# Kernel tuning notes

Hardware: AMD Instinct MI355X
Metric: run time of the kernel (lower is better)

The kernel has to match this reference:

```python
import jax, jax.numpy as jnp
import numpy as np

EPS = 1e-6

def _ln(x, g, b):
    mu = jnp.mean(x, -1, keepdims=True)
    var = jnp.mean((x - mu) ** 2, -1, keepdims=True)
    return (x - mu) / jnp.sqrt(var + EPS) * g + b

def _attn(q, k, v, nh, mask=None):
    B, Lq, H = q.shape
    Lk = k.shape[1]
    dh = H // nh
    q = q.reshape(B, Lq, nh, dh).transpose(0, 2, 1, 3)
    k = k.reshape(B, Lk, nh, dh).transpose(0, 2, 1, 3)
    v = v.reshape(B, Lk, nh, dh).transpose(0, 2, 1, 3)
    s = jnp.einsum('bhqd,bhkd->bhqk', q, k) * (1.0 / np.float32(np.sqrt(dh)))
    if mask is not None:
        s = jnp.where(mask, jnp.float32(-1e30), s)
    a = jax.nn.softmax(s, axis=-1)
    o = jnp.einsum('bhqk,bhkd->bhqd', a, v)
    return o.transpose(0, 2, 1, 3).reshape(B, Lq, H)

def _forward(byte_seq, patch_boundaries, emb, g_ln1_g, g_ln1_b, g_wqkv, g_bqkv, g_wo, g_bo,
             g_ln2_g, g_ln2_b, g_w1, g_b1, g_w2, g_b2, fn_g, fn_b,
             ca_ln_g, ca_ln_b, ca_wqkv, ca_bqkv, ca_wo, ca_bo, head_w, head_b,
             n_heads=16, ca_heads=8):
    B, S = byte_seq.shape
    P = patch_boundaries.shape[1]
    H = emb.shape[1]
    x = emb[byte_seq]  # [B,S,H] byte embeddings (local encoder)
    # ragged patch pooling: patch id of byte i = #boundaries <= i (BabylonIndex patches)
    pos = jnp.arange(S)
    pid = jax.vmap(lambda bd: jnp.searchsorted(bd, pos, side='right'))(patch_boundaries)
    pid = jnp.clip(pid, 0, P - 1)
    seg = lambda vals, ids: jax.ops.segment_sum(vals, ids, num_segments=P)
    sums = jax.vmap(seg)(x, pid)                                  # [B,P,H]
    cnts = jax.vmap(seg)(jnp.ones((B, S), x.dtype), pid)          # [B,P]
    patches = sums / jnp.maximum(cnts, 1.0)[..., None]            # mean-pooled patch reps
    causal = jnp.triu(jnp.ones((P, P), bool), 1)
    def layer(h, p):
        l1g, l1b, wqkv, bqkv, wo, bo, l2g, l2b, w1, b1, w2, b2 = p
        n = _ln(h, l1g, l1b)
        q, k, v = jnp.split(n @ wqkv + bqkv, 3, axis=-1)
        h = h + _attn(q, k, v, n_heads, causal) @ wo + bo
        n2 = _ln(h, l2g, l2b)
        h = h + jax.nn.gelu(n2 @ w1 + b1, approximate=False) @ w2 + b2
        return h, None
    patches, _ = jax.lax.scan(layer, patches, (g_ln1_g, g_ln1_b, g_wqkv, g_bqkv, g_wo, g_bo,
                                               g_ln2_g, g_ln2_b, g_w1, g_b1, g_w2, g_b2))
    patches = _ln(patches, fn_g, fn_b)  # GlobalLatentTransformer.final_norm
    # cross attention: byte queries attend to global patch representations
    qn = _ln(x, ca_ln_g, ca_ln_b)
    kvn = _ln(patches, ca_ln_g, ca_ln_b)
    q = qn @ ca_wqkv[:, :H] + ca_bqkv[:H]
    k = kvn @ ca_wqkv[:, H:2 * H] + ca_bqkv[H:2 * H]
    v = kvn @ ca_wqkv[:, 2 * H:] + ca_bqkv[2 * H:]
    h = x + _attn(q, k, v, ca_heads) @ ca_wo + ca_bo
    return h @ head_w + head_b  # [B,S,256] next-byte logits

def setup_inputs() -> dict:
    key = jax.random.key(0)
    ks = jax.random.split(key, 16)
    B, S, P, H, L, V = 2, 4096, 256, 1024, 4, 256
    std = 0.02
    d = {}
    d['byte_seq'] = jax.random.randint(ks[0], (B, S), 0, V, dtype=jnp.int32)
    d['patch_boundaries'] = jnp.sort(jax.random.randint(ks[1], (B, P), 1, S, dtype=jnp.int32), axis=-1)
    d['emb'] = jax.random.normal(ks[2], (V, H), jnp.float32) * std
    d['g_ln1_g'] = jnp.ones((L, H), jnp.float32)
    d['g_ln1_b'] = jnp.zeros((L, H), jnp.float32)
    d['g_wqkv'] = jax.random.normal(ks[3], (L, H, 3 * H), jnp.float32) * std
    d['g_bqkv'] = jnp.zeros((L, 3 * H), jnp.float32)
    d['g_wo'] = jax.random.normal(ks[4], (L, H, H), jnp.float32) * std
    d['g_bo'] = jnp.zeros((L, H), jnp.float32)
    d['g_ln2_g'] = jnp.ones((L, H), jnp.float32)
    d['g_ln2_b'] = jnp.zeros((L, H), jnp.float32)
    d['g_w1'] = jax.random.normal(ks[5], (L, H, 4 * H), jnp.float32) * std
    d['g_b1'] = jnp.zeros((L, 4 * H), jnp.float32)
    d['g_w2'] = jax.random.normal(ks[6], (L, 4 * H, H), jnp.float32) * std
    d['g_b2'] = jnp.zeros((L, H), jnp.float32)
    d['fn_g'] = jnp.ones((H,), jnp.float32)
    d['fn_b'] = jnp.zeros((H,), jnp.float32)
    d['ca_ln_g'] = jnp.ones((H,), jnp.float32)
    d['ca_ln_b'] = jnp.zeros((H,), jnp.float32)
    d['ca_wqkv'] = jax.random.normal(ks[7], (H, 3 * H), jnp.float32) * std
    d['ca_bqkv'] = jnp.zeros((3 * H,), jnp.float32)
    d['ca_wo'] = jax.random.normal(ks[8], (H, H), jnp.float32) * std
    d['ca_bo'] = jnp.zeros((H,), jnp.float32)
    d['head_w'] = jax.random.normal(ks[9], (H, V), jnp.float32) * std
    d['head_b'] = jnp.zeros((V,), jnp.float32)
    return d

def reference(byte_seq, patch_boundaries, emb, g_ln1_g, g_ln1_b, g_wqkv, g_bqkv, g_wo, g_bo,
              g_ln2_g, g_ln2_b, g_w1, g_b1, g_w2, g_b2, fn_g, fn_b,
              ca_ln_g, ca_ln_b, ca_wqkv, ca_bqkv, ca_wo, ca_bo, head_w, head_b):
    return _forward(byte_seq, patch_boundaries, emb, g_ln1_g, g_ln1_b, g_wqkv, g_bqkv, g_wo, g_bo,
                    g_ln2_g, g_ln2_b, g_w1, g_b1, g_w2, g_b2, fn_g, fn_b,
                    ca_ln_g, ca_ln_b, ca_wqkv, ca_bqkv, ca_wo, ca_bo, head_w, head_b)
```

## Files before the change

### kernel.cpp

```cpp
#include <hip/hip_runtime.h>
#include <hip/hip_bf16.h>
#include <math.h>

#define Hdim 1024
#define Bsz  2
#define Slen 4096
#define Pn   256
#define NLAY 4

typedef __attribute__((ext_vector_type(8))) __bf16 bfrag;
typedef __attribute__((ext_vector_type(4))) float  f32x4;

__device__ __forceinline__ float gelu_exact(float x) {
  return 0.5f * x * (1.0f + erff(x * 0.70710678118654752f));
}
__device__ __forceinline__ short f2b(float x) {
  __hip_bfloat16 h = __float2bfloat16(x);
  return *reinterpret_cast<short*>(&h);
}

__global__ void embed_kernel(const int* __restrict__ seq, const float* __restrict__ emb,
                             float* __restrict__ x) {
  int row = blockIdx.x;
  int tid = threadIdx.x;
  int tok = seq[row];
  float4 v = *(const float4*)(emb + (size_t)tok * Hdim + tid * 4);
  *(float4*)(x + (size_t)row * Hdim + tid * 4) = v;
}

__global__ void pid_kernel(const int* __restrict__ bounds, int* __restrict__ pid) {
  int i = blockIdx.x * 256 + threadIdx.x;
  int b = i >> 12;
  int s = i & (Slen - 1);
  const int* bd = bounds + b * Pn;
  int lo = 0, hi = Pn;
  while (lo < hi) { int m = (lo + hi) >> 1; if (bd[m] <= s) lo = m + 1; else hi = m; }
  pid[i] = min(lo, Pn - 1);
}

__global__ void pool_kernel(const float* __restrict__ x, const int* __restrict__ pid,
                            float* __restrict__ patches) {
  int bp = blockIdx.x;
  int b = bp >> 8;
  int p = bp & (Pn - 1);
  const int* pv = pid + b * Slen;
  int lo = 0, hi = Slen;
  while (lo < hi) { int m = (lo + hi) >> 1; if (pv[m] < p) lo = m + 1; else hi = m; }
  int start = lo;
  lo = 0; hi = Slen;
  while (lo < hi) { int m = (lo + hi) >> 1; if (pv[m] < p + 1) lo = m + 1; else hi = m; }
  int end = lo;
  int tid = threadIdx.x;
  float4 acc = {0.f, 0.f, 0.f, 0.f};
  for (int s = start; s < end; ++s) {
    float4 xv = *(const float4*)(x + ((size_t)(b * Slen + s)) * Hdim + tid * 4);
    acc.x += xv.x; acc.y += xv.y; acc.z += xv.z; acc.w += xv.w;
  }
  float cnt = (float)(end - start);
  float r = 1.0f / fmaxf(cnt, 1.0f);
  float4 o = {acc.x * r, acc.y * r, acc.z * r, acc.w * r};
  *(float4*)(patches + (size_t)bp * Hdim + tid * 4) = o;
}

template<int OBF>
__global__ void ln_kernel(const float* __restrict__ in, const float* __restrict__ g,
                          const float* __restrict__ bvec, void* __restrict__ outv) {
  int row = blockIdx.x;
  int tid = threadIdx.x;
  const float* xr = in + (size_t)row * Hdim;
  float4 v = *(const float4*)(xr + tid * 4);
  float s  = v.x + v.y + v.z + v.w;
  float ss = v.x * v.x + v.y * v.y + v.z * v.z + v.w * v.w;
#pragma unroll
  for (int off = 32; off; off >>= 1) { s += __shfl_xor(s, off); ss += __shfl_xor(ss, off); }
  __shared__ float rs[4], rss[4];
  int wid = tid >> 6;
  if ((tid & 63) == 0) { rs[wid] = s; rss[wid] = ss; }
  __syncthreads();
  float tot  = rs[0] + rs[1] + rs[2] + rs[3];
  float tot2 = rss[0] + rss[1] + rss[2] + rss[3];
  float mu = tot * (1.0f / Hdim);
  float var = tot2 * (1.0f / Hdim) - mu * mu;
  float rstd = rsqrtf(var + 1e-6f);
  float4 gg = *(const float4*)(g + tid * 4);
  float4 bb = *(const float4*)(bvec + tid * 4);
  float4 r;
  r.x = (v.x - mu) * rstd * gg.x + bb.x;
  r.y = (v.y - mu) * rstd * gg.y + bb.y;
  r.z = (v.z - mu) * rstd * gg.z + bb.z;
  r.w = (v.w - mu) * rstd * gg.w + bb.w;
  if (OBF) {
    short4 o; o.x = f2b(r.x); o.y = f2b(r.y); o.z = f2b(r.z); o.w = f2b(r.w);
    *(short4*)((short*)outv + (size_t)row * Hdim + tid * 4) = o;
  } else {
    *(float4*)((float*)outv + (size_t)row * Hdim + tid * 4) = r;
  }
}

__global__ void wconv_kernel(const float* __restrict__ in, short* __restrict__ out,
                             int ldin, int K, size_t in_lstride, size_t out_lstride) {
  int z = blockIdx.z;
  const float* src = in + (size_t)z * in_lstride;
  short* dst = out + (size_t)z * out_lstride;
  int n0 = blockIdx.x * 32, k0 = blockIdx.y * 32;
  int tx = threadIdx.x & 31, ty = threadIdx.x >> 5;
  __shared__ float t[32][33];
#pragma unroll
  for (int i = 0; i < 4; i++)
    t[ty + 8 * i][tx] = src[(size_t)(k0 + ty + 8 * i) * ldin + n0 + tx];
  __syncthreads();
#pragma unroll
  for (int i = 0; i < 4; i++)
    dst[(size_t)(n0 + ty + 8 * i) * K + k0 + tx] = f2b(t[tx][ty + 8 * i]);
}

__global__ void vt_kernel(const float* __restrict__ in, short* __restrict__ out) {
  int bh = blockIdx.z; int h = bh & 7; int b = bh >> 3;
  int kk0 = blockIdx.x * 32, d0 = blockIdx.y * 32;
  int tx = threadIdx.x & 31, ty = threadIdx.x >> 5;
  __shared__ float t[32][33];
  const float* src = in + (size_t)b * Pn * Hdim + h * 128;
#pragma unroll
  for (int i = 0; i < 4; i++)
    t[ty + 8 * i][tx] = src[(size_t)(kk0 + ty + 8 * i) * Hdim + d0 + tx];
  __syncthreads();
  short* dst = out + (size_t)bh * 128 * 256;
#pragma unroll
  for (int i = 0; i < 4; i++)
    dst[(size_t)(d0 + ty + 8 * i) * 256 + kk0 + tx] = f2b(t[tx][ty + 8 * i]);
}

__global__ void vtg_kernel(const short* __restrict__ qkvb, short* __restrict__ out) {
  int bh = blockIdx.z; int h = bh & 15; int b = bh >> 4;
  int kk0 = blockIdx.x * 32, d0 = blockIdx.y * 32;
  int tx = threadIdx.x & 31, ty = threadIdx.x >> 5;
  __shared__ short t[32][33];
  const short* src = qkvb + (size_t)b * Pn * 3072 + 2048 + h * 64;
#pragma unroll
  for (int i = 0; i < 4; i++)
    t[ty + 8 * i][tx] = src[(size_t)(kk0 + ty + 8 * i) * 3072 + d0 + tx];
  __syncthreads();
  short* dst = out + (size_t)bh * 64 * 256;
#pragma unroll
  for (int i = 0; i < 4; i++)
    dst[(size_t)(d0 + ty + 8 * i) * 256 + kk0 + tx] = t[tx][ty + 8 * i];
}

template<int EPI, int OBF>
__launch_bounds__(256)
__global__ void gemm_bf16(const short* __restrict__ A, const short* __restrict__ Bt,
                          const float* __restrict__ bias, const float* __restrict__ res,
                          void* __restrict__ Cv, int ldc, int K) {
  __shared__ short As[128][40];
  __shared__ short Bs[128][40];
  int tid = threadIdx.x;
  int n0 = blockIdx.x * 128, m0 = blockIdx.y * 128;
  int lr = tid >> 2;
  int lc = (tid & 3) * 8;
  int wid = tid >> 6, lane = tid & 63;
  int wm = (wid & 1) * 64, wn = (wid >> 1) * 64;
  int quad = lane >> 4, l16 = lane & 15;
  f32x4 acc[4][4];
#pragma unroll
  for (int i = 0; i < 4; i++)
#pragma unroll
    for (int j = 0; j < 4; j++) acc[i][j] = (f32x4){0.f, 0.f, 0.f, 0.f};

  for (int k0 = 0; k0 < K; k0 += 32) {
    int4 av0 = *(const int4*)(A + (size_t)(m0 + lr) * K + k0 + lc);
    int4 av1 = *(const int4*)(A + (size_t)(m0 + lr + 64) * K + k0 + lc);
    int4 bv0 = *(const int4*)(Bt + (size_t)(n0 + lr) * K + k0 + lc);
    int4 bv1 = *(const int4*)(Bt + (size_t)(n0 + lr + 64) * K + k0 + lc);
    __syncthreads();
    *(int4*)&As[lr][lc] = av0;  *(int4*)&As[lr + 64][lc] = av1;
    *(int4*)&Bs[lr][lc] = bv0;  *(int4*)&Bs[lr + 64][lc] = bv1;
    __syncthreads();
    bfrag af[4], bfv[4];
#pragma unroll
    for (int mi = 0; mi < 4; mi++)
      af[mi] = *reinterpret_cast<const bfrag*>(&As[wm + mi * 16 + l16][quad * 8]);
#pragma unroll
    for (int ni = 0; ni < 4; ni++)
      bfv[ni] = *reinterpret_cast<const bfrag*>(&Bs[wn + ni * 16 + l16][quad * 8]);
#pragma unroll
    for (int mi = 0; mi < 4; mi++)
#pragma unroll
      for (int ni = 0; ni < 4; ni++)
        acc[mi][ni] = __builtin_amdgcn_mfma_f32_16x16x32_bf16(af[mi], bfv[ni], acc[mi][ni], 0, 0, 0);
  }

#pragma unroll
  for (int mi = 0; mi < 4; mi++)
#pragma unroll
    for (int ni = 0; ni < 4; ni++) {
      int c = n0 + wn + ni * 16 + l16;
      float bsv = bias[c];
#pragma unroll
      for (int reg = 0; reg < 4; reg++) {
        int r = m0 + wm + mi * 16 + quad * 4 + reg;
        float v = acc[mi][ni][reg] + bsv;
        if (EPI == 1) v = gelu_exact(v);
        if (EPI == 2) v += res[(size_t)r * ldc + c];
        if (OBF) ((short*)Cv)[(size_t)r * ldc + c] = f2b(v);
        else     ((float*)Cv)[(size_t)r * ldc + c] = v;
      }
    }
}

template<int EPI, int OBF>
__launch_bounds__(256)
__global__ void gemm_bf16_64(const short* __restrict__ A, const short* __restrict__ Bt,
                             const float* __restrict__ bias, const float* __restrict__ res,
                             void* __restrict__ Cv, int ldc, int K) {
  __shared__ short As[64][40];
  __shared__ short Bs[64][40];
  int tid = threadIdx.x;
  int n0 = blockIdx.x * 64, m0 = blockIdx.y * 64;
  int lr = tid >> 2;
  int lc = (tid & 3) * 8;
  int wid = tid >> 6, lane = tid & 63;
  int wm = (wid & 1) * 32, wn = (wid >> 1) * 32;
  int quad = lane >> 4, l16 = lane & 15;
  f32x4 acc[2][2];
#pragma unroll
  for (int i = 0; i < 2; i++)
#pragma unroll
    for (int j = 0; j < 2; j++) acc[i][j] = (f32x4){0.f, 0.f, 0.f, 0.f};

  for (int k0 = 0; k0 < K; k0 += 32) {
    int4 av = *(const int4*)(A + (size_t)(m0 + lr) * K + k0 + lc);
    int4 bv = *(const int4*)(Bt + (size_t)(n0 + lr) * K + k0 + lc);
    __syncthreads();
    *(int4*)&As[lr][lc] = av;
    *(int4*)&Bs[lr][lc] = bv;
    __syncthreads();
    bfrag af[2], bfv[2];
#pragma unroll
    for (int mi = 0; mi < 2; mi++)
      af[mi] = *reinterpret_cast<const bfrag*>(&As[wm + mi * 16 + l16][quad * 8]);
#pragma unroll
    for (int ni = 0; ni < 2; ni++)
      bfv[ni] = *reinterpret_cast<const bfrag*>(&Bs[wn + ni * 16 + l16][quad * 8]);
#pragma unroll
    for (int mi = 0; mi < 2; mi++)
#pragma unroll
      for (int ni = 0; ni < 2; ni++)
        acc[mi][ni] = __builtin_amdgcn_mfma_f32_16x16x32_bf16(af[mi], bfv[ni], acc[mi][ni], 0, 0, 0);
  }

#pragma unroll
  for (int mi = 0; mi < 2; mi++)
#pragma unroll
    for (int ni = 0; ni < 2; ni++) {
      int c = n0 + wn + ni * 16 + l16;
      float bsv = bias[c];
#pragma unroll
      for (int reg = 0; reg < 4; reg++) {
        int r = m0 + wm + mi * 16 + quad * 4 + reg;
        float v = acc[mi][ni][reg] + bsv;
        if (EPI == 1) v = gelu_exact(v);
        if (EPI == 2) v += res[(size_t)r * ldc + c];
        if (OBF) ((short*)Cv)[(size_t)r * ldc + c] = f2b(v);
        else     ((float*)Cv)[(size_t)r * ldc + c] = v;
      }
    }
}

__launch_bounds__(256)
__global__ void gemm_splitk(const short* __restrict__ A, const short* __restrict__ Bt,
                            float* __restrict__ part, int K, int Ks) {
  __shared__ short As[64][40];
  __shared__ short Bs[64][40];
  int tid = threadIdx.x;
  int n0 = blockIdx.x * 64, m0 = blockIdx.y * 64, s = blockIdx.z;
  int kbase = s * Ks;
  int lr = tid >> 2;
  int lc = (tid & 3) * 8;
  int wid = tid >> 6, lane = tid & 63;
  int wm = (wid & 1) * 32, wn = (wid >> 1) * 32;
  int quad = lane >> 4, l16 = lane & 15;
  f32x4 acc[2][2];
#pragma unroll
  for (int i = 0; i < 2; i++)
#pragma unroll
    for (int j = 0; j < 2; j++) acc[i][j] = (f32x4){0.f, 0.f, 0.f, 0.f};

  for (int k0 = kbase; k0 < kbase + Ks; k0 += 32) {
    int4 av = *(const int4*)(A + (size_t)(m0 + lr) * K + k0 + lc);
    int4 bv = *(const int4*)(Bt + (size_t)(n0 + lr) * K + k0 + lc);
    __syncthreads();
    *(int4*)&As[lr][lc] = av;
    *(int4*)&Bs[lr][lc] = bv;
    __syncthreads();
    bfrag af[2], bfv[2];
#pragma unroll
    for (int mi = 0; mi < 2; mi++)
      af[mi] = *reinterpret_cast<const bfrag*>(&As[wm + mi * 16 + l16][quad * 8]);
#pragma unroll
    for (int ni = 0; ni < 2; ni++)
      bfv[ni] = *reinterpret_cast<const bfrag*>(&Bs[wn + ni * 16 + l16][quad * 8]);
#pragma unroll
    for (int mi = 0; mi < 2; mi++)
#pragma unroll
      for (int ni = 0; ni < 2; ni++)
        acc[mi][ni] = __builtin_amdgcn_mfma_f32_16x16x32_bf16(af[mi], bfv[ni], acc[mi][ni], 0, 0, 0);
  }

#pragma unroll
  for (int mi = 0; mi < 2; mi++)
#pragma unroll
    for (int ni = 0; ni < 2; ni++) {
      int c = n0 + wn + ni * 16 + l16;
#pragma unroll
      for (int reg = 0; reg < 4; reg++) {
        int r = m0 + wm + mi * 16 + quad * 4 + reg;
        part[(size_t)s * 524288 + (size_t)r * 1024 + c] = acc[mi][ni][reg];
      }
    }
}

__global__ void w2red_kernel(const float* __restrict__ part, const float* __restrict__ bias,
                             float* __restrict__ patches) {
  int i = (blockIdx.x * 256 + threadIdx.x) * 4;
  float4 v = *(const float4*)(part + i);
#pragma unroll
  for (int s = 1; s < 4; s++) {
    float4 p = *(const float4*)(part + (size_t)s * 524288 + i);
    v.x += p.x; v.y += p.y; v.z += p.z; v.w += p.w;
  }
  int c = i & 1023;
  float4 bv = *(const float4*)(bias + c);
  float4 rv = *(const float4*)(patches + i);
  v.x += bv.x + rv.x; v.y += bv.y + rv.y; v.z += bv.z + rv.z; v.w += bv.w + rv.w;
  *(float4*)(patches + i) = v;
}

__launch_bounds__(256)
__global__ void attn_global3(const short* __restrict__ qkvb, const short* __restrict__ vtg,
                             short* __restrict__ outp) {
  int qt = blockIdx.x;
  int bh = blockIdx.y; int h = bh & 15, b = bh >> 4;
  int tid = threadIdx.x;
  int wid = tid >> 6, lane = tid & 63;
  int quad = lane >> 4, l16 = lane & 15;
  int q0 = qt * 64 + wid * 16;
  __shared__ short KV[64 * 72];
  __shared__ short Pl[4][16][264];
  const short* qrow = qkvb + ((size_t)(b * Pn + q0 + l16)) * 3072 + h * 64 + quad * 8;
  bfrag qf[2];
#pragma unroll
  for (int kd = 0; kd < 2; kd++) qf[kd] = *(const bfrag*)(qrow + kd * 32);
  f32x4 sacc[16];
#pragma unroll
  for (int n = 0; n < 16; n++) sacc[n] = (f32x4){0.f, 0.f, 0.f, 0.f};
  int cr = tid >> 2, cc = (tid & 3) * 16;
#pragma unroll
  for (int kc = 0; kc < 4; kc++) {
    if (kc <= qt) {
      const short* ksrc = qkvb + ((size_t)(b * Pn + kc * 64 + cr)) * 3072 + 1024 + h * 64 + cc;
      int4 v0 = *(const int4*)(ksrc);
      int4 v1 = *(const int4*)(ksrc + 8);
      __syncthreads();
      *(int4*)&KV[cr * 72 + cc] = v0;
      *(int4*)&KV[cr * 72 + cc + 8] = v1;
      __syncthreads();
#pragma unroll
      for (int n = 0; n < 4; n++)
#pragma unroll
        for (int kd = 0; kd < 2; kd++) {
          bfrag kf = *(const bfrag*)&KV[(n * 16 + l16) * 72 + kd * 32 + quad * 8];
          sacc[kc * 4 + n] = __builtin_amdgcn_mfma_f32_16x16x32_bf16(qf[kd], kf, sacc[kc * 4 + n], 0, 0, 0);
        }
    }
  }
  int nfr = (qt + 1) * 4;
  const float scale = 0.125f;
  float mx[4] = {-1e30f, -1e30f, -1e30f, -1e30f};
#pragma unroll
  for (int n = 0; n < 16; n++) {
    if (n < nfr) {
      int col = n * 16 + l16;
#pragma unroll
      for (int r = 0; r < 4; r++)
        if (col <= q0 + quad * 4 + r) mx[r] = fmaxf(mx[r], sacc[n][r]);
    }
  }
#pragma unroll
  for (int off = 1; off < 16; off <<= 1)
#pragma unroll
    for (int r = 0; r < 4; r++) mx[r] = fmaxf(mx[r], __shfl_xor(mx[r], off));
  float ls[4] = {0.f, 0.f, 0.f, 0.f};
#pragma unroll
  for (int n = 0; n < 16; n++) {
    if (n < nfr) {
      int col = n * 16 + l16;
#pragma unroll
      for (int r = 0; r < 4; r++) {
        float p = (col <= q0 + quad * 4 + r) ? __expf((sacc[n][r] - mx[r]) * scale) : 0.f;
        Pl[wid][quad * 4 + r][col] = f2b(p);
        ls[r] += p;
      }
    }
  }
#pragma unroll
  for (int off = 1; off < 16; off <<= 1)
#pragma unroll
    for (int r = 0; r < 4; r++) ls[r] += __shfl_xor(ls[r], off);
  float rl[4];
#pragma unroll
  for (int r = 0; r < 4; r++) rl[r] = 1.0f / ls[r];

  f32x4 oacc[4];
#pragma unroll
  for (int n = 0; n < 4; n++) oacc[n] = (f32x4){0.f, 0.f, 0.f, 0.f};
#pragma unroll
  for (int kc = 0; kc < 4; kc++) {
    if (kc <= qt) {
      const short* vsrc = vtg + (size_t)bh * 64 * 256 + cr * 256 + kc * 64 + cc;
      int4 v0 = *(const int4*)(vsrc);
      int4 v1 = *(const int4*)(vsrc + 8);
      __syncthreads();
      *(int4*)&KV[cr * 72 + cc] = v0;
      *(int4*)&KV[cr * 72 + cc + 8] = v1;
      __syncthreads();
#pragma unroll
      for (int kk = 0; kk < 2; kk++) {
        bfrag pa = *(const bfrag*)&Pl[wid][l16][kc * 64 + kk * 32 + quad * 8];
#pragma unroll
        for (int n = 0; n < 4; n++) {
          bfrag vf = *(const bfrag*)&KV[(n * 16 + l16) * 72 + kk * 32 + quad * 8];
          oacc[n] = __builtin_amdgcn_mfma_f32_16x16x32_bf16(pa, vf, oacc[n], 0, 0, 0);
        }
      }
    }
  }
#pragma unroll
  for (int n = 0; n < 4; n++)
#pragma unroll
    for (int r = 0; r < 4; r++)
      outp[(size_t)(b * Pn + q0 + quad * 4 + r) * Hdim + h * 64 + n * 16 + l16] = f2b(oacc[n][r] * rl[r]);
}

__launch_bounds__(256)
__global__ void attn_cross4(const short* __restrict__ q, const short* __restrict__ k,
                            const short* __restrict__ vt, short* __restrict__ outp) {
  int bh = blockIdx.y; int h = bh & 7, b = bh >> 3;
  int tid = threadIdx.x;
  int wid = tid >> 6, lane = tid & 63;
  int quad = lane >> 4, l16 = lane & 15;
  int q0 = blockIdx.x * 64 + wid * 16;
  __shared__ short KV[9216];
  __shared__ short Pl[4][16][264];
  const short* qrow = q + ((size_t)(b * Slen + q0 + l16)) * Hdim + h * 128 + quad * 8;
  bfrag qf[4];
#pragma unroll
  for (int kd = 0; kd < 4; kd++) qf[kd] = *(const bfrag*)(qrow + kd * 32);
  f32x4 sacc[16];
#pragma unroll
  for (int n = 0; n < 16; n++) sacc[n] = (f32x4){0.f, 0.f, 0.f, 0.f};

  int cr4 = tid >> 2, cc4 = (tid & 3) * 32;
#pragma unroll
  for (int kc = 0; kc < 4; kc++) {
    const short* ksrc = k + ((size_t)(b * Pn + kc * 64 + cr4)) * Hdim + h * 128 + cc4;
    int4 v0 = *(const int4*)(ksrc);
    int4 v1 = *(const int4*)(ksrc + 8);
    int4 v2 = *(const int4*)(ksrc + 16);
    int4 v3 = *(const int4*)(ksrc + 24);
    __syncthreads();
    *(int4*)&KV[cr4 * 136 + cc4]      = v0;
    *(int4*)&KV[cr4 * 136 + cc4 + 8]  = v1;
    *(int4*)&KV[cr4 * 136 + cc4 + 16] = v2;
    *(int4*)&KV[cr4 * 136 + cc4 + 24] = v3;
    __syncthreads();
#pragma unroll
    for (int n = 0; n < 4; n++)
#pragma unroll
      for (int kd = 0; kd < 4; kd++) {
        bfrag kf = *(const bfrag*)&KV[(n * 16 + l16) * 136 + kd * 32 + quad * 8];
        sacc[kc * 4 + n] = __builtin_amdgcn_mfma_f32_16x16x32_bf16(qf[kd], kf, sacc[kc * 4 + n], 0, 0, 0);
      }
  }

  const float scale = 0.088388347648318447f;
  float mx[4] = {-1e30f, -1e30f, -1e30f, -1e30f};
#pragma unroll
  for (int n = 0; n < 16; n++)
#pragma unroll
    for (int r = 0; r < 4; r++) mx[r] = fmaxf(mx[r], sacc[n][r]);
#pragma unroll
  for (int off = 1; off < 16; off <<= 1)
#pragma unroll
    for (int r = 0; r < 4; r++) mx[r] = fmaxf(mx[r], __shfl_xor(mx[r], off));
  float ls[4] = {0.f, 0.f, 0.f, 0.f};
#pragma unroll
  for (int n = 0; n < 16; n++)
#pragma unroll
    for (int r = 0; r < 4; r++) {
      float p = __expf((sacc[n][r] - mx[r]) * scale);
      Pl[wid][quad * 4 + r][n * 16 + l16] = f2b(p);
      ls[r] += p;
    }
#pragma unroll
  for (int off = 1; off < 16; off <<= 1)
#pragma unroll
    for (int r = 0; r < 4; r++) ls[r] += __shfl_xor(ls[r], off);
  float rl[4];
#pragma unroll
  for (int r = 0; r < 4; r++) rl[r] = 1.0f / ls[r];

  f32x4 oacc[8];
#pragma unroll
  for (int n = 0; n < 8; n++) oacc[n] = (f32x4){0.f, 0.f, 0.f, 0.f};
  int cr2 = tid >> 1, cc2 = (tid & 1) * 32;
#pragma unroll
  for (int kc = 0; kc < 4; kc++) {
    const short* vsrc = vt + (size_t)bh * 32768 + cr2 * 256 + kc * 64 + cc2;
    int4 v0 = *(const int4*)(vsrc);
    int4 v1 = *(const int4*)(vsrc + 8);
    int4 v2 = *(const int4*)(vsrc + 16);
    int4 v3 = *(const int4*)(vsrc + 24);
    __syncthreads();
    *(int4*)&KV[cr2 * 72 + cc2]      = v0;
    *(int4*)&KV[cr2 * 72 + cc2 + 8]  = v1;
    *(int4*)&KV[cr2 * 72 + cc2 + 16] = v2;
    *(int4*)&KV[cr2 * 72 + cc2 + 24] = v3;
    __syncthreads();
#pragma unroll
    for (int kk = 0; kk < 2; kk++) {
      bfrag pa = *(const bfrag*)&Pl[wid][l16][kc * 64 + kk * 32 + quad * 8];
#pragma unroll
      for (int n = 0; n < 8; n++) {
        bfrag vf = *(const bfrag*)&KV[(n * 16 + l16) * 72 + kk * 32 + quad * 8];
        oacc[n] = __builtin_amdgcn_mfma_f32_16x16x32_bf16(pa, vf, oacc[n], 0, 0, 0);
      }
    }
  }
#pragma unroll
  for (int n = 0; n < 8; n++)
#pragma unroll
    for (int r = 0; r < 4; r++)
      outp[(size_t)(b * Slen + q0 + quad * 4 + r) * Hdim + h * 128 + n * 16 + l16] = f2b(oacc[n][r] * rl[r]);
}

extern "C" void kernel_launch(void* const* d_in, const int* in_sizes, int n_in,
                              void* d_out, int out_size, void* d_ws, size_t ws_size,
                              hipStream_t stream) {
  const int*   byte_seq = (const int*)d_in[0];
  const int*   pbound   = (const int*)d_in[1];
  const float* emb      = (const float*)d_in[2];
  const float* g_ln1_g  = (const float*)d_in[3];
  const float* g_ln1_b  = (const float*)d_in[4];
  const float* g_wqkv   = (const float*)d_in[5];
  const float* g_bqkv   = (const float*)d_in[6];
  const float* g_wo     = (const float*)d_in[7];
  const float* g_bo     = (const float*)d_in[8];
  const float* g_ln2_g  = (const float*)d_in[9];
  const float* g_ln2_b  = (const float*)d_in[10];
  const float* g_w1     = (const float*)d_in[11];
  const float* g_b1     = (const float*)d_in[12];
  const float* g_w2     = (const float*)d_in[13];
  const float* g_b2     = (const float*)d_in[14];
  const float* fn_g     = (const float*)d_in[15];
  const float* fn_b     = (const float*)d_in[16];
  const float* ca_ln_g  = (const float*)d_in[17];
  const float* ca_ln_b  = (const float*)d_in[18];
  const float* ca_wqkv  = (const float*)d_in[19];
  const float* ca_bqkv  = (const float*)d_in[20];
  const float* ca_wo    = (const float*)d_in[21];
  const float* ca_bo    = (const float*)d_in[22];
  const float* head_w   = (const float*)d_in[23];
  const float* head_b   = (const float*)d_in[24];
  float* out = (float*)d_out;

  float* x       = (float*)d_ws;
  float* patches = x + 8388608;
  float* vbuf    = patches + 524288;
  float* w2part  = vbuf + 524288;
  int*   pid     = (int*)(w2part + 2097152);
  short* nbuf    = (short*)(pid + 8192);
  short* attn_o  = nbuf + 524288;
  short* mid     = attn_o + 524288;
  short* qn      = mid + 2097152;
  short* qb      = qn + 8388608;
  short* xb      = qb + 8388608;
  short* kb      = xb + 8388608;
  short* vt      = kb + 524288;
  short* qkvb    = vt + 524288;
  short* vtg     = qkvb + 1572864;
  short* wqkv_t  = vtg + 524288;
  short* wo_t    = wqkv_t + 12582912;
  short* w1_t    = wo_t + 4194304;
  short* w2_t    = w1_t + 16777216;
  short* caq_t   = w2_t + 16777216;
  short* cak_t   = caq_t + 1048576;
  short* cav_t   = cak_t + 1048576;
  short* cawo_t  = cav_t + 1048576;
  short* head_t  = cawo_t + 1048576;
  short* caout   = qn;

  embed_kernel<<<Bsz * Slen, 256, 0, stream>>>(byte_seq, emb, x);
  pid_kernel<<<(Bsz * Slen) / 256, 256, 0, stream>>>(pbound, pid);
  pool_kernel<<<Bsz * Pn, 256, 0, stream>>>(x, pid, patches);

  wconv_kernel<<<dim3(96, 32, 4), 256, 0, stream>>>(g_wqkv, wqkv_t, 3072, 1024, 3145728, 3145728);
  wconv_kernel<<<dim3(32, 32, 4), 256, 0, stream>>>(g_wo, wo_t, 1024, 1024, 1048576, 1048576);
  wconv_kernel<<<dim3(128, 32, 4), 256, 0, stream>>>(g_w1, w1_t, 4096, 1024, 4194304, 4194304);
  wconv_kernel<<<dim3(32, 128, 4), 256, 0, stream>>>(g_w2, w2_t, 1024, 4096, 4194304, 4194304);
  wconv_kernel<<<dim3(32, 32, 3), 256, 0, stream>>>(ca_wqkv, caq_t, 3072, 1024, 1024, 1048576);
  wconv_kernel<<<dim3(32, 32, 1), 256, 0, stream>>>(ca_wo, cawo_t, 1024, 1024, 0, 0);
  wconv_kernel<<<dim3(8, 32, 1), 256, 0, stream>>>(head_w, head_t, 256, 1024, 0, 0);

  for (int l = 0; l < NLAY; ++l) {
    ln_kernel<1><<<Bsz * Pn, 256, 0, stream>>>(patches, g_ln1_g + l * Hdim, g_ln1_b + l * Hdim, nbuf);
    gemm_bf16_64<0, 1><<<dim3(48, 8), 256, 0, stream>>>(
        nbuf, wqkv_t + (size_t)l * 3145728, g_bqkv + l * 3072, nullptr, qkvb, 3072, 1024);
    vtg_kernel<<<dim3(8, 2, 32), 256, 0, stream>>>(qkvb, vtg);
    attn_global3<<<dim3(4, 32), 256, 0, stream>>>(qkvb, vtg, attn_o);
    gemm_bf16_64<2, 0><<<dim3(16, 8), 256, 0, stream>>>(
        attn_o, wo_t + (size_t)l * 1048576, g_bo + l * Hdim, patches, patches, 1024, 1024);
    ln_kernel<1><<<Bsz * Pn, 256, 0, stream>>>(patches, g_ln2_g + l * Hdim, g_ln2_b + l * Hdim, nbuf);
    gemm_bf16_64<1, 1><<<dim3(64, 8), 256, 0, stream>>>(
        nbuf, w1_t + (size_t)l * 4194304, g_b1 + l * 4096, nullptr, mid, 4096, 1024);
    gemm_splitk<<<dim3(16, 8, 4), 256, 0, stream>>>(
        mid, w2_t + (size_t)l * 4194304, w2part, 4096, 1024);
    w2red_kernel<<<512, 256, 0, stream>>>(w2part, g_b2 + l * Hdim, patches);
  }

  ln_kernel<0><<<Bsz * Pn, 256, 0, stream>>>(patches, fn_g, fn_b, patches);
  ln_kernel<1><<<Bsz * Pn, 256, 0, stream>>>(patches, ca_ln_g, ca_ln_b, nbuf);

  gemm_bf16_64<0, 1><<<dim3(16, 8), 256, 0, stream>>>(
      nbuf, cak_t, ca_bqkv + 1024, nullptr, kb, 1024, 1024);
  gemm_bf16_64<0, 0><<<dim3(16, 8), 256, 0, stream>>>(
      nbuf, cav_t, ca_bqkv + 2048, nullptr, vbuf, 1024, 1024);
  vt_kernel<<<dim3(8, 4, 16), 256, 0, stream>>>(vbuf, vt);

  ln_kernel<1><<<Bsz * Slen, 256, 0, stream>>>(x, ca_ln_g, ca_ln_b, qn);
  gemm_bf16<0, 1><<<dim3(8, 64), 256, 0, stream>>>(
      qn, caq_t, ca_bqkv, nullptr, qb, 1024, 1024);

  attn_cross4<<<dim3(64, 16), 256, 0, stream>>>(qb, kb, vt, caout);

  gemm_bf16<2, 1><<<dim3(8, 64), 256, 0, stream>>>(
      caout, cawo_t, ca_bo, x, xb, 1024, 1024);

  gemm_bf16_64<0, 0><<<dim3(4, 128), 256, 0, stream>>>(
      xb, head_t, head_b, nullptr, out, 256, 1024);
}
```

Before: 850.4 us.

## Load GEMM tiles directly to LDS and fuse cross-attn LayerNorm into embedding

All three bf16 GEMM kernels now stage A and B tiles with global_load_lds (direct global-to-LDS 16-byte loads) into unpadded 32-wide LDS rows, so the data no longer passes through registers. The byte-level LayerNorm for cross-attention queries is folded into the embedding kernel, which removes a separate pass over the 8192x1024 activation. Dropping the LDS padding can raise bank conflicts on fragment reads, and the LayerNorm now uses a single-pass E[x^2]-mu^2 variance, which is slightly less numerically robust.

```diff
diff --git a/kernel.cpp b/kernel.cpp
--- a/kernel.cpp
+++ b/kernel.cpp
@@ -18,14 +18,41 @@
   __hip_bfloat16 h = __float2bfloat16(x);
   return *reinterpret_cast<short*>(&h);
 }
-
-__global__ void embed_kernel(const int* __restrict__ seq, const float* __restrict__ emb,
-                             float* __restrict__ x) {
+__device__ __forceinline__ void gload16(const short* g, short* l) {
+  __builtin_amdgcn_global_load_lds(
+      (const __attribute__((address_space(1))) unsigned int*)g,
+      (__attribute__((address_space(3))) unsigned int*)l, 16, 0, 0);
+}
+
+__global__ void embed_ln_kernel(const int* __restrict__ seq, const float* __restrict__ emb,
+                                const float* __restrict__ g, const float* __restrict__ bvec,
+                                float* __restrict__ x, short* __restrict__ qn) {
   int row = blockIdx.x;
   int tid = threadIdx.x;
   int tok = seq[row];
   float4 v = *(const float4*)(emb + (size_t)tok * Hdim + tid * 4);
   *(float4*)(x + (size_t)row * Hdim + tid * 4) = v;
+  float s  = v.x + v.y + v.z + v.w;
+  float ss = v.x * v.x + v.y * v.y + v.z * v.z + v.w * v.w;
+#pragma unroll
+  for (int off = 32; off; off >>= 1) { s += __shfl_xor(s, off); ss += __shfl_xor(ss, off); }
+  __shared__ float rs[4], rss[4];
+  int wid = tid >> 6;
+  if ((tid & 63) == 0) { rs[wid] = s; rss[wid] = ss; }
+  __syncthreads();
+  float tot  = rs[0] + rs[1] + rs[2] + rs[3];
+  float tot2 = rss[0] + rss[1] + rss[2] + rss[3];
+  float mu = tot * (1.0f / Hdim);
+  float var = tot2 * (1.0f / Hdim) - mu * mu;
+  float rstd = rsqrtf(var + 1e-6f);
+  float4 gg = *(const float4*)(g + tid * 4);
+  float4 bb = *(const float4*)(bvec + tid * 4);
+  short4 o;
+  o.x = f2b((v.x - mu) * rstd * gg.x + bb.x);
+  o.y = f2b((v.y - mu) * rstd * gg.y + bb.y);
+  o.z = f2b((v.z - mu) * rstd * gg.z + bb.z);
+  o.w = f2b((v.w - mu) * rstd * gg.w + bb.w);
+  *(short4*)(qn + (size_t)row * Hdim + tid * 4) = o;
 }
 
 __global__ void pid_kernel(const int* __restrict__ bounds, int* __restrict__ pid) {
@@ -151,8 +178,8 @@
 __global__ void gemm_bf16(const short* __restrict__ A, const short* __restrict__ Bt,
                           const float* __restrict__ bias, const float* __restrict__ res,
                           void* __restrict__ Cv, int ldc, int K) {
-  __shared__ short As[128][40];
-  __shared__ short Bs[128][40];
+  __shared__ short As[128 * 32];
+  __shared__ short Bs[128 * 32];
   int tid = threadIdx.x;
   int n0 = blockIdx.x * 128, m0 = blockIdx.y * 128;
   int lr = tid >> 2;
@@ -166,22 +193,29 @@
 #pragma unroll
     for (int j = 0; j < 4; j++) acc[i][j] = (f32x4){0.f, 0.f, 0.f, 0.f};
 
+  const short* ga0 = A + (size_t)(m0 + lr) * K + lc;
+  const short* ga1 = A + (size_t)(m0 + lr + 64) * K + lc;
+  const short* gb0 = Bt + (size_t)(n0 + lr) * K + lc;
+  const short* gb1 = Bt + (size_t)(n0 + lr + 64) * K + lc;
+  short* la0 = As + tid * 8;
+  short* la1 = As + 2048 + tid * 8;
+  short* lb0 = Bs + tid * 8;
+  short* lb1 = Bs + 2048 + tid * 8;
+
   for (int k0 = 0; k0 < K; k0 += 32) {
-    int4 av0 = *(const int4*)(A + (size_t)(m0 + lr) * K + k0 + lc);
-    int4 av1 = *(const int4*)(A + (size_t)(m0 + lr + 64) * K + k0 + lc);
-    int4 bv0 = *(const int4*)(Bt + (size_t)(n0 + lr) * K + k0 + lc);
-    int4 bv1 = *(const int4*)(Bt + (size_t)(n0 + lr + 64) * K + k0 + lc);
-    __syncthreads();
-    *(int4*)&As[lr][lc] = av0;  *(int4*)&As[lr + 64][lc] = av1;
-    *(int4*)&Bs[lr][lc] = bv0;  *(int4*)&Bs[lr + 64][lc] = bv1;
+    __syncthreads();
+    gload16(ga0 + k0, la0);
+    gload16(ga1 + k0, la1);
+    gload16(gb0 + k0, lb0);
+    gload16(gb1 + k0, lb1);
     __syncthreads();
     bfrag af[4], bfv[4];
 #pragma unroll
     for (int mi = 0; mi < 4; mi++)
-      af[mi] = *reinterpret_cast<const bfrag*>(&As[wm + mi * 16 + l16][quad * 8]);
+      af[mi] = *reinterpret_cast<const bfrag*>(&As[(wm + mi * 16 + l16) * 32 + quad * 8]);
 #pragma unroll
     for (int ni = 0; ni < 4; ni++)
-      bfv[ni] = *reinterpret_cast<const bfrag*>(&Bs[wn + ni * 16 + l16][quad * 8]);
+      bfv[ni] = *reinterpret_cast<const bfrag*>(&Bs[(wn + ni * 16 + l16) * 32 + quad * 8]);
 #pragma unroll
     for (int mi = 0; mi < 4; mi++)
 #pragma unroll
@@ -212,8 +246,8 @@
 __global__ void gemm_bf16_64(const short* __restrict__ A, const short* __restrict__ Bt,
                              const float* __restrict__ bias, const float* __restrict__ res,
                              void* __restrict__ Cv, int ldc, int K) {
-  __shared__ short As[64][40];
-  __shared__ short Bs[64][40];
+  __shared__ short As[64 * 32];
+  __shared__ short Bs[64 * 32];
   int tid = threadIdx.x;
   int n0 = blockIdx.x * 64, m0 = blockIdx.y * 64;
   int lr = tid >> 2;
@@ -227,20 +261,23 @@
 #pragma unroll
     for (int j = 0; j < 2; j++) acc[i][j] = (f32x4){0.f, 0.f, 0.f, 0.f};
 
+  const short* ga = A + (size_t)(m0 + lr) * K + lc;
+  const short* gb = Bt + (size_t)(n0 + lr) * K + lc;
+  short* la = As + tid * 8;
+  short* lb = Bs + tid * 8;
+
   for (int k0 = 0; k0 < K; k0 += 32) {
-    int4 av = *(const int4*)(A + (size_t)(m0 + lr) * K + k0 + lc);
-    int4 bv = *(const int4*)(Bt + (size_t)(n0 + lr) * K + k0 + lc);
-    __syncthreads();
-    *(int4*)&As[lr][lc] = av;
-    *(int4*)&Bs[lr][lc] = bv;
+    __syncthreads();
+    gload16(ga + k0, la);
+    gload16(gb + k0, lb);
     __syncthreads();
     bfrag af[2], bfv[2];
 #pragma unroll
     for (int mi = 0; mi < 2; mi++)
-      af[mi] = *reinterpret_cast<const bfrag*>(&As[wm + mi * 16 + l16][quad * 8]);
+      af[mi] = *reinterpret_cast<const bfrag*>(&As[(wm + mi * 16 + l16) * 32 + quad * 8]);
 #pragma unroll
     for (int ni = 0; ni < 2; ni++)
-      bfv[ni] = *reinterpret_cast<const bfrag*>(&Bs[wn + ni * 16 + l16][quad * 8]);
+      bfv[ni] = *reinterpret_cast<const bfrag*>(&Bs[(wn + ni * 16 + l16) * 32 + quad * 8]);
 #pragma unroll
     for (int mi = 0; mi < 2; mi++)
 #pragma unroll
@@ -269,8 +306,8 @@
 __launch_bounds__(256)
 __global__ void gemm_splitk(const short* __restrict__ A, const short* __restrict__ Bt,
                             float* __restrict__ part, int K, int Ks) {
-  __shared__ short As[64][40];
-  __shared__ short Bs[64][40];
+  __shared__ short As[64 * 32];
+  __shared__ short Bs[64 * 32];
   int tid = threadIdx.x;
   int n0 = blockIdx.x * 64, m0 = blockIdx.y * 64, s = blockIdx.z;
   int kbase = s * Ks;
@@ -285,20 +322,23 @@
 #pragma unroll
     for (int j = 0; j < 2; j++) acc[i][j] = (f32x4){0.f, 0.f, 0.f, 0.f};
 
+  const short* ga = A + (size_t)(m0 + lr) * K + lc;
+  const short* gb = Bt + (size_t)(n0 + lr) * K + lc;
+  short* la = As + tid * 8;
+  short* lb = Bs + tid * 8;
+
   for (int k0 = kbase; k0 < kbase + Ks; k0 += 32) {
-    int4 av = *(const int4*)(A + (size_t)(m0 + lr) * K + k0 + lc);
-    int4 bv = *(const int4*)(Bt + (size_t)(n0 + lr) * K + k0 + lc);
-    __syncthreads();
-    *(int4*)&As[lr][lc] = av;
-    *(int4*)&Bs[lr][lc] = bv;
+    __syncthreads();
+    gload16(ga + k0, la);
+    gload16(gb + k0, lb);
     __syncthreads();
     bfrag af[2], bfv[2];
 #pragma unroll
     for (int mi = 0; mi < 2; mi++)
-      af[mi] = *reinterpret_cast<const bfrag*>(&As[wm + mi * 16 + l16][quad * 8]);
+      af[mi] = *reinterpret_cast<const bfrag*>(&As[(wm + mi * 16 + l16) * 32 + quad * 8]);
 #pragma unroll
     for (int ni = 0; ni < 2; ni++)
-      bfv[ni] = *reinterpret_cast<const bfrag*>(&Bs[wn + ni * 16 + l16][quad * 8]);
+      bfv[ni] = *reinterpret_cast<const bfrag*>(&Bs[(wn + ni * 16 + l16) * 32 + quad * 8]);
 #pragma unroll
     for (int mi = 0; mi < 2; mi++)
 #pragma unroll
@@ -599,7 +639,7 @@
   short* head_t  = cawo_t + 1048576;
   short* caout   = qn;
 
-  embed_kernel<<<Bsz * Slen, 256, 0, stream>>>(byte_seq, emb, x);
+  embed_ln_kernel<<<Bsz * Slen, 256, 0, stream>>>(byte_seq, emb, ca_ln_g, ca_ln_b, x, qn);
   pid_kernel<<<(Bsz * Slen) / 256, 256, 0, stream>>>(pbound, pid);
   pool_kernel<<<Bsz * Pn, 256, 0, stream>>>(x, pid, patches);
 
@@ -636,7 +676,6 @@
       nbuf, cav_t, ca_bqkv + 2048, nullptr, vbuf, 1024, 1024);
   vt_kernel<<<dim3(8, 4, 16), 256, 0, stream>>>(vbuf, vt);
 
-  ln_kernel<1><<<Bsz * Slen, 256, 0, stream>>>(x, ca_ln_g, ca_ln_b, qn);
   gemm_bf16<0, 1><<<dim3(8, 64), 256, 0, stream>>>(
       qn, caq_t, ca_bqkv, nullptr, qb, 1024, 1024);
 
```

Result: faster. 826.3 us (-2.8%).
